# Optimization experiments

Hardware: AMD Instinct MI355X
Metric: run time of the kernel (lower is better)

The kernel has to match this reference:

```python
import jax, jax.numpy as jnp
import numpy as np

# ---- static config (matches init_kwargs) ----
L = 8          # multipath taps
DECAY = 4.0
N = 512        # batch
P = 1
M_SUB = 64     # opt.M
K_CP = 16      # opt.K
N_PILOT = 2
NS = 62
S = NS + N_PILOT            # 64  (OFDM, is_pb)
M = M_SUB + K_CP + N_PILOT  # 82
SMK = S * M                 # 5248
CARRIER = 3.6e9
SCS = 15e3
C_LIGHT = 3e8


def setup_inputs() -> dict:
    key = jax.random.key(0)
    k1, k2, k3, k4, k5 = jax.random.split(key, 5)
    eps = 1e-6
    return {
        "input_real": jax.random.normal(k1, (N, P, SMK), jnp.float32),
        "input_imag": jax.random.normal(k2, (N, P, SMK), jnp.float32),
        "ray_u": jax.random.uniform(k3, (N, P, L), jnp.float32, eps, 1.0 - eps),
        "angles_u": jax.random.uniform(k4, (L,), jnp.float32),
        "phase_u": jax.random.uniform(k5, (N, P, L, 1), jnp.float32),
        "velocity": 30,
        "Ns": NS,
    }


def _channel(input_real, input_imag, ray_u, angles_u, phase_u, velocity, Ns):
    S_ = Ns + N_PILOT  # == S
    two_pi = 2.0 * np.pi
    x = (input_real + 1j * input_imag).astype(jnp.complex64)

    # tap power profile and Rayleigh fading gains (rayleigh(u)=sqrt(-2 ln u))
    power = jnp.exp(-jnp.arange(L, dtype=jnp.float32) / DECAY)
    power = power / jnp.sum(power)
    cof = jnp.sqrt(power / 2.0) * jnp.sqrt(-2.0 * jnp.log(ray_u))  # (N,P,L)
    cof = -jnp.sort(-cof, axis=-1)  # descending sort

    # Doppler phase ramp: phases = (2*pi*cos(angle)*f_d + phi0) * t
    t = jnp.arange(S_, dtype=jnp.float32) / SCS  # (S,)
    fd = jnp.float32(velocity) / C_LIGHT * CARRIER
    doppler = two_pi * jnp.cos(angles_u * two_pi) * fd        # (L,)
    ph0 = doppler[None, None, :, None] + phase_u * two_pi      # (N,P,L,1)
    phases = ph0 * t[None, None, None, :]                      # (N,P,L,S)
    shift = jnp.exp(1j * phases).astype(jnp.complex64)
    cof_fin = cof[..., None].astype(jnp.complex64) * shift     # (N,P,L,S)

    # per-path time-varying gain applied to the OFDM grid
    xr = x.reshape(N, P, 1, S_, M)
    out = xr * cof_fin[..., None]                              # (N,P,L,S,M)

    # batch_conv1d with flipped eye / L == delay path l by l samples, scale 1/L
    T = S_ * M
    y = out.reshape(N, P, L, T)
    yp = jnp.pad(y, ((0, 0), (0, 0), (0, 0), (L - 1, 0)))      # (N,P,L,T+L-1)
    idx = (L - 1) - jnp.arange(L)[:, None] + jnp.arange(T)[None, :]  # (L,T)
    yd = jnp.take_along_axis(yp, idx[None, None], axis=-1) / L

    output = jnp.sum(yd, axis=2).reshape(N, P, SMK)            # complex64
    H_t = jnp.sum(cof_fin, axis=2).squeeze()                   # (N,S) complex64
    return output, H_t


def reference(input_real, input_imag, ray_u, angles_u, phase_u, velocity, Ns):
    return _channel(input_real, input_imag, ray_u, angles_u, phase_u, velocity, Ns)
```

## Files before the change

kernel.cpp:

```cpp
#include <hip/hip_runtime.h>
#include <hip/hip_bf16.h>


#define CH_L 8
#define CH_N 512
#define CH_S 64
#define CH_M 82
#define CH_T 5248
#define GROUPS_N 656
#define CONV_BLOCKS 1312

#define TWO_PI 6.283185307179586f

__device__ __forceinline__ unsigned pack_bf16x2(float lo, float hi) {
    __hip_bfloat16 hl = __float2bfloat16(lo);
    __hip_bfloat16 hh = __float2bfloat16(hi);
    unsigned short ul = *reinterpret_cast<unsigned short*>(&hl);
    unsigned short uh = *reinterpret_cast<unsigned short*>(&hh);
    return (unsigned)ul | ((unsigned)uh << 16);
}

__global__ __launch_bounds__(64) void prep_kernel(
    const float* __restrict__ ray_u,
    const float* __restrict__ angles_u,
    const float* __restrict__ phase_u,
    const void*  __restrict__ vel_raw,
    float2*      __restrict__ cf_ws,
    __hip_bfloat16* __restrict__ out)
{
    const int n   = blockIdx.x;
    const int tid = threadIdx.x;

    __shared__ float s_c[CH_L];
    __shared__ float s_ph0[CH_L];

    if (tid < CH_L) {
        float psum = 0.0f;
        #pragma unroll
        for (int l = 0; l < CH_L; ++l) psum += __expf(-(float)l / 4.0f);
        float pw = __expf(-(float)tid / 4.0f);
        float u  = ray_u[n * CH_L + tid];
        s_c[tid] = sqrtf(pw / (2.0f * psum)) * sqrtf(-2.0f * __logf(u));
    }
    __syncthreads();
    if (tid == 0) {
        float c[CH_L];
        #pragma unroll
        for (int l = 0; l < CH_L; ++l) c[l] = s_c[l];
        for (int i = 1; i < CH_L; ++i) {
            float v = c[i];
            int j = i - 1;
            while (j >= 0 && c[j] < v) { c[j + 1] = c[j]; --j; }
            c[j + 1] = v;
        }
        #pragma unroll
        for (int l = 0; l < CH_L; ++l) s_c[l] = c[l];
    }
    __syncthreads();
    if (tid < CH_L) {
        const int   vi = *reinterpret_cast<const int*>(vel_raw);
        const float vf = *reinterpret_cast<const float*>(vel_raw);
        float vel;
        if (vi != 0 && vi > -1000000 && vi < 1000000) vel = (float)vi;
        else if (vf == vf && fabsf(vf) > 1e-3f && fabsf(vf) < 1e6f) vel = vf;
        else vel = 30.0f;
        const float fd = vel * (1.0f / 3.0e8f) * 3.6e9f;
        float ang = angles_u[tid] * TWO_PI;
        s_ph0[tid] = TWO_PI * __cosf(ang) * fd + phase_u[n * CH_L + tid] * TWO_PI;
    }
    __syncthreads();

    const float ts = (float)tid * (1.0f / 15000.0f);
    float hr = 0.0f, hi = 0.0f;
    #pragma unroll
    for (int l = 0; l < CH_L; ++l) {
        float sn, cs;
        __sincosf(s_ph0[l] * ts, &sn, &cs);
        float g = s_c[l];
        float2 v = make_float2(g * cs, g * sn);
        cf_ws[((size_t)n * CH_L + l) * CH_S + tid] = v;
        hr += v.x; hi += v.y;
    }
    size_t j = (size_t)CH_N * CH_T + (size_t)n * CH_S + tid;
    *reinterpret_cast<unsigned*>(&out[2 * j]) = pack_bf16x2(hi, hr);
}

__global__ __launch_bounds__(256) void conv_kernel(
    const float* __restrict__ xr,
    const float* __restrict__ xi,
    const float2* __restrict__ cf_ws,
    __hip_bfloat16* __restrict__ out)
{
    const int g  = blockIdx.x * 256 + threadIdx.x;
    const int n  = g / GROUPS_N;
    const int gg = g - n * GROUPS_N;
    const int t0 = gg << 3;

    const int s00 = t0 / CH_M;
    const int m00 = t0 - s00 * CH_M;
    const int sHi = s00 + ((m00 + 7) >= CH_M ? 1 : 0);
    int sLo = s00 - (m00 < 7 ? 1 : 0);
    if (sLo < 0) sLo = 0;

    const float2* cfn = cf_ws + (size_t)n * (CH_L * CH_S);
    float2 flo[CH_L], fhi[CH_L];
    #pragma unroll
    for (int l = 0; l < CH_L; ++l) {
        flo[l] = cfn[(l << 6) + sLo];
        fhi[l] = cfn[(l << 6) + sHi];
    }

    const float* xrn = xr + (size_t)n * CH_T;
    const float* xin = xi + (size_t)n * CH_T;

    float wr[16], wi[16];
    if (t0 == 0) {
        #pragma unroll
        for (int k = 0; k < 8; ++k) { wr[k] = 0.0f; wi[k] = 0.0f; }
        float4 a = *reinterpret_cast<const float4*>(xrn);
        float4 b = *reinterpret_cast<const float4*>(xrn + 4);
        wr[8]=a.x; wr[9]=a.y; wr[10]=a.z; wr[11]=a.w;
        wr[12]=b.x; wr[13]=b.y; wr[14]=b.z; wr[15]=b.w;
        a = *reinterpret_cast<const float4*>(xin);
        b = *reinterpret_cast<const float4*>(xin + 4);
        wi[8]=a.x; wi[9]=a.y; wi[10]=a.z; wi[11]=a.w;
        wi[12]=b.x; wi[13]=b.y; wi[14]=b.z; wi[15]=b.w;
    } else {
        const float* pr = xrn + t0 - 8;
        float4 a = *reinterpret_cast<const float4*>(pr);
        float4 b = *reinterpret_cast<const float4*>(pr + 4);
        float4 c = *reinterpret_cast<const float4*>(pr + 8);
        float4 d = *reinterpret_cast<const float4*>(pr + 12);
        wr[0]=a.x; wr[1]=a.y; wr[2]=a.z; wr[3]=a.w;
        wr[4]=b.x; wr[5]=b.y; wr[6]=b.z; wr[7]=b.w;
        wr[8]=c.x; wr[9]=c.y; wr[10]=c.z; wr[11]=c.w;
        wr[12]=d.x; wr[13]=d.y; wr[14]=d.z; wr[15]=d.w;
        const float* pi = xin + t0 - 8;
        a = *reinterpret_cast<const float4*>(pi);
        b = *reinterpret_cast<const float4*>(pi + 4);
        c = *reinterpret_cast<const float4*>(pi + 8);
        d = *reinterpret_cast<const float4*>(pi + 12);
        wi[0]=a.x; wi[1]=a.y; wi[2]=a.z; wi[3]=a.w;
        wi[4]=b.x; wi[5]=b.y; wi[6]=b.z; wi[7]=b.w;
        wi[8]=c.x; wi[9]=c.y; wi[10]=c.z; wi[11]=c.w;
        wi[12]=d.x; wi[13]=d.y; wi[14]=d.z; wi[15]=d.w;
    }

    float rr[8], ii[8];
    #pragma unroll
    for (int k = 0; k < 8; ++k) {
        int m = m00 + k;
        int cross = (m >= CH_M) ? 1 : 0;
        m -= cross * CH_M;
        const int  s0   = s00 + cross;
        const bool hi_t = (s0 == sHi);
        float ar = 0.0f, ai = 0.0f;
        #pragma unroll
        for (int l = 0; l < CH_L; ++l) {
            float2 cf = (hi_t && (m >= l)) ? fhi[l] : flo[l];
            float vr  = wr[8 + k - l];
            float vi2 = wi[8 + k - l];
            ar += vr * cf.x - vi2 * cf.y;
            ai += vr * cf.y + vi2 * cf.x;
        }
        rr[k] = ar * 0.125f;
        ii[k] = ai * 0.125f;
    }

    size_t base = 2 * ((size_t)n * CH_T + t0);
    uint4 v0, v1;
    v0.x = pack_bf16x2(ii[0], rr[0]); v0.y = pack_bf16x2(ii[1], rr[1]);
    v0.z = pack_bf16x2(ii[2], rr[2]); v0.w = pack_bf16x2(ii[3], rr[3]);
    v1.x = pack_bf16x2(ii[4], rr[4]); v1.y = pack_bf16x2(ii[5], rr[5]);
    v1.z = pack_bf16x2(ii[6], rr[6]); v1.w = pack_bf16x2(ii[7], rr[7]);
    *reinterpret_cast<uint4*>(&out[base])     = v0;
    *reinterpret_cast<uint4*>(&out[base + 8]) = v1;
}

extern "C" void kernel_launch(void* const* d_in, const int* in_sizes, int n_in,
                              void* d_out, int out_size, void* d_ws, size_t ws_size,
                              hipStream_t stream) {
    const float* xr       = (const float*)d_in[0];
    const float* xi       = (const float*)d_in[1];
    const float* ray_u    = (const float*)d_in[2];
    const float* angles_u = (const float*)d_in[3];
    const float* phase_u  = (const float*)d_in[4];
    const void*  velocity = d_in[5];

    __hip_bfloat16* out = (__hip_bfloat16*)d_out;
    float2* cf_ws = (float2*)d_ws;

    prep_kernel<<<CH_N, 64, 0, stream>>>(ray_u, angles_u, phase_u, velocity,
                                         cf_ws, out);
    conv_kernel<<<CONV_BLOCKS, 256, 0, stream>>>(xr, xi, cf_ws, out);
}
```

Measured before the change: 19.32 us.

## Fuse coefficient prep into conv kernel with per-block LDS coefficient tile

Merges the prep and conv kernels into one launch over a (batch, quarter) grid. Each block recomputes the sorted fading gains and the 17-symbol Doppler coefficient slice it needs into shared memory, replacing the global workspace round-trip and the serial insertion sort with a parallel rank sort. This removes a kernel launch and the inter-kernel dependency. In exchange, only 164 of 256 threads do convolution work, and each block redoes the gain computation.

```diff
diff --git a/kernel.cpp b/kernel.cpp
--- a/kernel.cpp
+++ b/kernel.cpp
@@ -7,8 +7,9 @@
 #define CH_S 64
 #define CH_M 82
 #define CH_T 5248
-#define GROUPS_N 656
-#define CONV_BLOCKS 1312
+#define QSPLIT 4
+#define GROUPS_PER_BLK 164
+#define TILE_SLOTS 17
 
 #define TWO_PI 6.283185307179586f
 
@@ -20,19 +21,23 @@
     return (unsigned)ul | ((unsigned)uh << 16);
 }
 
-__global__ __launch_bounds__(64) void prep_kernel(
+__global__ __launch_bounds__(256) void channel_fused(
+    const float* __restrict__ xr,
+    const float* __restrict__ xi,
     const float* __restrict__ ray_u,
     const float* __restrict__ angles_u,
     const float* __restrict__ phase_u,
     const void*  __restrict__ vel_raw,
-    float2*      __restrict__ cf_ws,
     __hip_bfloat16* __restrict__ out)
 {
     const int n   = blockIdx.x;
+    const int q   = blockIdx.y;
     const int tid = threadIdx.x;
 
-    __shared__ float s_c[CH_L];
-    __shared__ float s_ph0[CH_L];
+    __shared__ float  s_raw[CH_L];
+    __shared__ float  s_srt[CH_L];
+    __shared__ float  s_ph0[CH_L];
+    __shared__ float2 tile[CH_L][TILE_SLOTS];
 
     if (tid < CH_L) {
         float psum = 0.0f;
@@ -40,24 +45,8 @@
         for (int l = 0; l < CH_L; ++l) psum += __expf(-(float)l / 4.0f);
         float pw = __expf(-(float)tid / 4.0f);
         float u  = ray_u[n * CH_L + tid];
-        s_c[tid] = sqrtf(pw / (2.0f * psum)) * sqrtf(-2.0f * __logf(u));
-    }
-    __syncthreads();
-    if (tid == 0) {
-        float c[CH_L];
-        #pragma unroll
-        for (int l = 0; l < CH_L; ++l) c[l] = s_c[l];
-        for (int i = 1; i < CH_L; ++i) {
-            float v = c[i];
-            int j = i - 1;
-            while (j >= 0 && c[j] < v) { c[j + 1] = c[j]; --j; }
-            c[j + 1] = v;
-        }
-        #pragma unroll
-        for (int l = 0; l < CH_L; ++l) s_c[l] = c[l];
-    }
-    __syncthreads();
-    if (tid < CH_L) {
+        s_raw[tid] = sqrtf(pw / (2.0f * psum)) * sqrtf(-2.0f * __logf(u));
+
         const int   vi = *reinterpret_cast<const int*>(vel_raw);
         const float vf = *reinterpret_cast<const float*>(vel_raw);
         float vel;
@@ -65,49 +54,62 @@
         else if (vf == vf && fabsf(vf) > 1e-3f && fabsf(vf) < 1e6f) vel = vf;
         else vel = 30.0f;
         const float fd = vel * (1.0f / 3.0e8f) * 3.6e9f;
-        float ang = angles_u[tid] * TWO_PI;
-        s_ph0[tid] = TWO_PI * __cosf(ang) * fd + phase_u[n * CH_L + tid] * TWO_PI;
+        s_ph0[tid] = TWO_PI * __cosf(angles_u[tid] * TWO_PI) * fd
+                   + phase_u[n * CH_L + tid] * TWO_PI;
+    }
+    __syncthreads();
+    if (tid < CH_L) {
+        float mine = s_raw[tid];
+        int rank = 0;
+        #pragma unroll
+        for (int j = 0; j < CH_L; ++j) {
+            float o = s_raw[j];
+            rank += (o > mine) || (o == mine && j < tid);
+        }
+        s_srt[rank] = mine;
+    }
+    __syncthreads();
+    if (tid < CH_L * TILE_SLOTS) {
+        int l    = tid / TILE_SLOTS;
+        int slot = tid - l * TILE_SLOTS;
+        int s    = 16 * q - 1 + slot;
+        float2 v = make_float2(0.0f, 0.0f);
+        if (s >= 0) {
+            float sn, cs;
+            __sincosf(s_ph0[l] * ((float)s * (1.0f / 15000.0f)), &sn, &cs);
+            float g = s_srt[l];
+            v = make_float2(g * cs, g * sn);
+        }
+        tile[l][slot] = v;
     }
     __syncthreads();
 
-    const float ts = (float)tid * (1.0f / 15000.0f);
-    float hr = 0.0f, hi = 0.0f;
-    #pragma unroll
-    for (int l = 0; l < CH_L; ++l) {
-        float sn, cs;
-        __sincosf(s_ph0[l] * ts, &sn, &cs);
-        float g = s_c[l];
-        float2 v = make_float2(g * cs, g * sn);
-        cf_ws[((size_t)n * CH_L + l) * CH_S + tid] = v;
-        hr += v.x; hi += v.y;
+    if (tid < 16) {
+        float hr = 0.0f, hi = 0.0f;
+        #pragma unroll
+        for (int l = 0; l < CH_L; ++l) {
+            float2 v = tile[l][tid + 1];
+            hr += v.x; hi += v.y;
+        }
+        size_t j = (size_t)CH_N * CH_T + (size_t)n * CH_S + 16 * q + tid;
+        *reinterpret_cast<unsigned*>(&out[2 * j]) = pack_bf16x2(hi, hr);
     }
-    size_t j = (size_t)CH_N * CH_T + (size_t)n * CH_S + tid;
-    *reinterpret_cast<unsigned*>(&out[2 * j]) = pack_bf16x2(hi, hr);
-}
 
-__global__ __launch_bounds__(256) void conv_kernel(
-    const float* __restrict__ xr,
-    const float* __restrict__ xi,
-    const float2* __restrict__ cf_ws,
-    __hip_bfloat16* __restrict__ out)
-{
-    const int g  = blockIdx.x * 256 + threadIdx.x;
-    const int n  = g / GROUPS_N;
-    const int gg = g - n * GROUPS_N;
-    const int t0 = gg << 3;
+    if (tid >= GROUPS_PER_BLK) return;
 
+    const int t0  = 1312 * q + (tid << 3);
     const int s00 = t0 / CH_M;
     const int m00 = t0 - s00 * CH_M;
     const int sHi = s00 + ((m00 + 7) >= CH_M ? 1 : 0);
-    int sLo = s00 - (m00 < 7 ? 1 : 0);
-    if (sLo < 0) sLo = 0;
+    const int sLo = s00 - (m00 < 7 ? 1 : 0);
+    const int slotLo = sLo - 16 * q + 1;
+    const int slotHi = sHi - 16 * q + 1;
 
-    const float2* cfn = cf_ws + (size_t)n * (CH_L * CH_S);
     float2 flo[CH_L], fhi[CH_L];
     #pragma unroll
     for (int l = 0; l < CH_L; ++l) {
-        flo[l] = cfn[(l << 6) + sLo];
-        fhi[l] = cfn[(l << 6) + sHi];
+        flo[l] = tile[l][slotLo];
+        fhi[l] = tile[l][slotHi];
     }
 
     const float* xrn = xr + (size_t)n * CH_T;
@@ -152,8 +154,7 @@
         int m = m00 + k;
         int cross = (m >= CH_M) ? 1 : 0;
         m -= cross * CH_M;
-        const int  s0   = s00 + cross;
-        const bool hi_t = (s0 == sHi);
+        const bool hi_t = ((s00 + cross) == sHi);
         float ar = 0.0f, ai = 0.0f;
         #pragma unroll
         for (int l = 0; l < CH_L; ++l) {
@@ -188,9 +189,8 @@
     const void*  velocity = d_in[5];
 
     __hip_bfloat16* out = (__hip_bfloat16*)d_out;
-    float2* cf_ws = (float2*)d_ws;
 
-    prep_kernel<<<CH_N, 64, 0, stream>>>(ray_u, angles_u, phase_u, velocity,
-                                         cf_ws, out);
-    conv_kernel<<<CONV_BLOCKS, 256, 0, stream>>>(xr, xi, cf_ws, out);
+    dim3 grid(CH_N, QSPLIT);
+    channel_fused<<<grid, 256, 0, stream>>>(xr, xi, ray_u, angles_u, phase_u,
+                                            velocity, out);
 }
```

New measurement: 17.34 us. -10.3%, faster.
